# Kernel tuning notes

Hardware: AMD Instinct MI355X
Metric: run time of the kernel (lower is better)

## Reference

```python
import jax, jax.numpy as jnp
import numpy as np

NUM_GRAPHS = 64  # number of graphs in the batch for global_mean_pool
BN_EPS = 1e-5


def setup_inputs() -> dict:
    key = jax.random.key(0)
    ks = jax.random.split(key, 8)
    N, E, D, H, O = 100000, 1600000, 128, 128, 32
    x = jax.random.normal(ks[0], (N, D), dtype=jnp.float32)
    edge_index = jax.random.randint(ks[1], (2, E), 0, N, dtype=jnp.int64)
    batch = jnp.sort(jax.random.randint(ks[2], (N,), 0, NUM_GRAPHS, dtype=jnp.int64))
    s = 1.0 / np.sqrt(D)
    W0 = (jax.random.normal(ks[3], (D, H), dtype=jnp.float32) * s)
    b0 = jnp.zeros((H,), jnp.float32)
    g0 = jnp.ones((H,), jnp.float32)
    be0 = jnp.zeros((H,), jnp.float32)
    W1 = (jax.random.normal(ks[4], (H, H), dtype=jnp.float32) * s)
    b1 = jnp.zeros((H,), jnp.float32)
    g1 = jnp.ones((H,), jnp.float32)
    be1 = jnp.zeros((H,), jnp.float32)
    Wfc = (jax.random.normal(ks[5], (H, O), dtype=jnp.float32) * s)
    bfc = jnp.zeros((O,), jnp.float32)
    return dict(x=x, edge_index=edge_index, batch=batch,
                W0=W0, b0=b0, g0=g0, be0=be0,
                W1=W1, b1=b1, g1=g1, be1=be1,
                Wfc=Wfc, bfc=bfc)


def reference(x, edge_index, batch, W0, b0, g0, be0, W1, b1, g1, be1, Wfc, bfc):
    N = x.shape[0]
    loops = jnp.arange(N, dtype=edge_index.dtype)
    src = jnp.concatenate([edge_index[0], loops])  # [E+N]
    dst = jnp.concatenate([edge_index[1], loops])
    # GCN symmetric normalization on A + I
    deg = jax.ops.segment_sum(jnp.ones_like(dst, jnp.float32), dst, num_segments=N)
    dinv = jnp.where(deg > 0, jax.lax.rsqrt(deg), 0.0)
    norm = dinv[src] * dinv[dst]  # [E+N]

    def gcn_layer(h, W, b):
        h = h @ W                                   # [N, H] transform first (PyG GCNConv)
        msg = h[src] * norm[:, None]                # gather + scale
        agg = jax.ops.segment_sum(msg, dst, num_segments=N)  # scatter-add
        return agg + b

    def bn_relu(h, g, be):  # BatchNorm1d (batch stats, biased var) + ReLU
        mu = h.mean(axis=0)
        var = h.var(axis=0)
        return jax.nn.relu((h - mu) * jax.lax.rsqrt(var + BN_EPS) * g + be)

    h = bn_relu(gcn_layer(x, W0, b0), g0, be0)
    h = bn_relu(gcn_layer(h, W1, b1), g1, be1)

    # global_mean_pool over graph assignment
    cnt = jax.ops.segment_sum(jnp.ones((N,), jnp.float32), batch, num_segments=NUM_GRAPHS)
    pooled = jax.ops.segment_sum(h, batch, num_segments=NUM_GRAPHS)
    pooled = pooled / jnp.maximum(cnt, 1.0)[:, None]
    return pooled @ Wfc + bfc  # [NUM_GRAPHS, out_dim]
```

## Files before the change

kernel.cpp:

```cpp
#include <hip/hip_runtime.h>

typedef short bf16x8 __attribute__((ext_vector_type(8)));
typedef float f32x4 __attribute__((ext_vector_type(4)));

#define NBLK 512
#define NSTAT 512

__device__ __forceinline__ unsigned short f2bf(float f) {
    unsigned u = __float_as_uint(f);
    u += 0x7fffu + ((u >> 16) & 1u);
    return (unsigned short)(u >> 16);
}
__device__ __forceinline__ float bflo(unsigned u) { return __uint_as_float(u << 16); }
__device__ __forceinline__ float bfhi(unsigned u) { return __uint_as_float(u & 0xffff0000u); }


__global__ __launch_bounds__(256) void kb_count(const int* __restrict__ dst, int E, int nb,
                                                int chunk, int* __restrict__ counts) {
    __shared__ int h[512];
    for (int i = threadIdx.x; i < 512; i += 256) h[i] = 0;
    __syncthreads();
    int e0 = blockIdx.x * chunk, e1 = min(e0 + chunk, E);
    for (int e = e0 + threadIdx.x; e < e1; e += 256) atomicAdd(&h[dst[e] >> 8], 1);
    __syncthreads();
    for (int b = threadIdx.x; b < nb; b += 256) counts[b * NBLK + blockIdx.x] = h[b];
}

__global__ __launch_bounds__(NBLK) void kb_offsets(int* __restrict__ counts,
                                                   int* __restrict__ total) {
    __shared__ int s[NBLK];
    int b = blockIdx.x, t = threadIdx.x;
    int v = counts[b * NBLK + t];
    s[t] = v; __syncthreads();
    for (int off = 1; off < NBLK; off <<= 1) {
        int x = (t >= off) ? s[t - off] : 0;
        __syncthreads();
        s[t] += x;
        __syncthreads();
    }
    counts[b * NBLK + t] = s[t] - v;
    if (t == NBLK - 1) total[b] = s[t];
}

__global__ __launch_bounds__(512) void kb_base(const int* __restrict__ in, int nb,
                                               int* __restrict__ outb) {
    __shared__ int s[512];
    int t = threadIdx.x;
    int v = (t < nb) ? in[t] : 0;
    s[t] = v; __syncthreads();
    for (int off = 1; off < 512; off <<= 1) {
        int x = (t >= off) ? s[t - off] : 0;
        __syncthreads();
        s[t] += x;
        __syncthreads();
    }
    if (t < nb) outb[t] = s[t] - v;
}

__global__ __launch_bounds__(NBLK) void kb_scatter(const int* __restrict__ src,
                                                   const int* __restrict__ dst, int E, int nb,
                                                   int chunk,
                                                   const int* __restrict__ counts,
                                                   const int* __restrict__ bbase,
                                                   int2* __restrict__ rec) {
    __shared__ int cur[512];
    int t = threadIdx.x;
    if (t < nb) cur[t] = bbase[t] + counts[t * NBLK + blockIdx.x];
    __syncthreads();
    int e0 = blockIdx.x * chunk, e1 = min(e0 + chunk, E);
    for (int e = e0 + t; e < e1; e += NBLK) {
        int s = src[e], d = dst[e];
        int pos = atomicAdd(&cur[d >> 8], 1);
        rec[pos] = make_int2(s, d);
    }
}

__global__ __launch_bounds__(256) void kb_deg(const int2* __restrict__ rec,
                                              const int* __restrict__ bbase,
                                              const int* __restrict__ total,
                                              int* __restrict__ deg,
                                              float* __restrict__ dinv,
                                              int* __restrict__ padsum, int N) {
    __shared__ int dc[256];
    int b = blockIdx.x, t = threadIdx.x;
    dc[t] = 0; __syncthreads();
    int r0 = bbase[b], r1 = r0 + total[b];
    for (int i = r0 + t; i < r1; i += 256) atomicAdd(&dc[rec[i].y & 255], 1);
    __syncthreads();
    int gn = b * 256 + t;
    int d = dc[t];
    int pd = (gn < N) ? ((d + 7) & ~7) : 0;
    if (gn < N) {
        deg[gn] = d;
        dinv[gn] = rsqrtf((float)(d + 1));
    }
    __syncthreads();
    dc[t] = pd; __syncthreads();
    for (int off = 128; off > 0; off >>= 1) {
        if (t < off) dc[t] += dc[t + off];
        __syncthreads();
    }
    if (t == 0) padsum[b] = dc[0];
}

__global__ __launch_bounds__(256) void kb_place(const int2* __restrict__ rec,
                                                const int* __restrict__ bbase,
                                                const int* __restrict__ total,
                                                const int* __restrict__ bucketBase,
                                                const int* __restrict__ deg,
                                                const float* __restrict__ dinv,
                                                int2* __restrict__ csr,
                                                int2* __restrict__ rowdeg, int N) {
    __shared__ int sc[256];
    __shared__ int cur[256];
    int b = blockIdx.x, t = threadIdx.x;
    int gn = b * 256 + t;
    int d = (gn < N) ? deg[gn] : 0;
    int pd = (d + 7) & ~7;
    sc[t] = pd; __syncthreads();
    for (int off = 1; off < 256; off <<= 1) {
        int x = (t >= off) ? sc[t - off] : 0;
        __syncthreads();
        sc[t] += x;
        __syncthreads();
    }
    int rp = bucketBase[b] + sc[t] - pd;
    if (gn < N) rowdeg[gn] = make_int2(rp, pd);
    cur[t] = rp;
    __syncthreads();
    int r0 = bbase[b], r1 = r0 + total[b];
    for (int i = r0 + t; i < r1; i += 256) {
        int2 rc = rec[i];
        int pos = atomicAdd(&cur[rc.y & 255], 1);
        float w = dinv[rc.x] * dinv[rc.y];
        csr[pos] = make_int2(rc.x, __float_as_int(w));
    }
    __syncthreads();
    if (gn < N) {
        int end = cur[t];
        int pe = rp + pd;
        for (int i = end; i < pe; ++i) csr[i] = make_int2(0, 0);
    }
}

__global__ __launch_bounds__(256) void k_wprep(const float* __restrict__ W0,
                                               const float* __restrict__ W1,
                                               unsigned short* __restrict__ W0t,
                                               unsigned short* __restrict__ W1t,
                                               float* __restrict__ pooled,
                                               int* __restrict__ gcnt) {
    int tt = blockIdx.x * 256 + threadIdx.x;
    pooled[tt] = 0.f;
    pooled[tt + 4096] = 0.f;
    if (tt < 64) gcnt[tt] = 0;
    const float* W = (tt < 2048) ? W0 : W1;
    unsigned short* Wt = (tt < 2048) ? W0t : W1t;
    int t = tt & 2047;
    int f = t >> 6, lane = t & 63;
    int kc = f >> 3, nt = f & 7;
    int kbase = kc * 32 + (lane >> 4) * 8;
    int n = nt * 16 + (lane & 15);
    unsigned short t8[8];
#pragma unroll
    for (int j = 0; j < 8; ++j) t8[j] = f2bf(W[(size_t)(kbase + j) * 128 + n]);
    unsigned short* o = &Wt[(size_t)t * 8];
    *(ushort4*)&o[0] = *(ushort4*)&t8[0];
    *(ushort4*)&o[4] = *(ushort4*)&t8[4];
}

__global__ __launch_bounds__(256) void k_gemm(const void* __restrict__ Xv,
                                              const unsigned short* __restrict__ Wt,
                                              const float* __restrict__ scale,
                                              const float* __restrict__ shift,
                                              unsigned short* __restrict__ Hout,
                                              int N, int xbf16) {
    __shared__ unsigned short sX[64 * 136];
    const int tid = threadIdx.x;
    const int rowBase = blockIdx.x * 64;

    if (!xbf16) {
        const float* X = (const float*)Xv;
#pragma unroll
        for (int i = 0; i < 8; ++i) {
            int f4 = tid + 256 * i;
            int r = f4 >> 5; int k4 = (f4 & 31) * 4;
            int gr = rowBase + r;
            float4 v = make_float4(0.f, 0.f, 0.f, 0.f);
            if (gr < N) v = *(const float4*)&X[(size_t)gr * 128 + k4];
            ushort4 p;
            p.x = f2bf(v.x); p.y = f2bf(v.y); p.z = f2bf(v.z); p.w = f2bf(v.w);
            *(ushort4*)&sX[r * 136 + k4] = p;
        }
    } else {
        const int4* X = (const int4*)Xv;
#pragma unroll
        for (int i = 0; i < 4; ++i) {
            int f8 = tid + 256 * i;
            int r = f8 >> 4; int k8 = (f8 & 15) * 8;
            int gr = rowBase + r;
            int4 u = make_int4(0, 0, 0, 0);
            if (gr < N) u = X[(size_t)gr * 16 + (f8 & 15)];
            float fv[8] = { bflo(u.x), bfhi(u.x), bflo(u.y), bfhi(u.y),
                            bflo(u.z), bfhi(u.z), bflo(u.w), bfhi(u.w) };
            unsigned short t8[8];
#pragma unroll
            for (int j = 0; j < 8; ++j)
                t8[j] = f2bf(fmaxf(fmaf(fv[j], scale[k8 + j], shift[k8 + j]), 0.f));
            *(ushort4*)&sX[r * 136 + k8]     = *(ushort4*)&t8[0];
            *(ushort4*)&sX[r * 136 + k8 + 4] = *(ushort4*)&t8[4];
        }
    }
    __syncthreads();

    const int lane = tid & 63, wave = tid >> 6;
    const int m = lane & 15, q = lane >> 4;
    const int rowOff = (wave * 16 + m) * 136 + q * 8;
    f32x4 acc[8];
#pragma unroll
    for (int nt = 0; nt < 8; ++nt) acc[nt] = (f32x4){0.f, 0.f, 0.f, 0.f};
    const bf16x8* WtF = (const bf16x8*)Wt;
#pragma unroll
    for (int kc = 0; kc < 4; ++kc) {
        bf16x8 xb = *(const bf16x8*)&sX[rowOff + kc * 32];
#pragma unroll
        for (int nt = 0; nt < 8; ++nt) {
            bf16x8 wa = WtF[(kc * 8 + nt) * 64 + lane];
            acc[nt] = __builtin_amdgcn_mfma_f32_16x16x32_bf16(wa, xb, acc[nt], 0, 0, 0);
        }
    }
    int grow = rowBase + wave * 16 + m;
    if (grow < N) {
#pragma unroll
        for (int nt = 0; nt < 8; ++nt) {
            ushort4 p;
            p.x = f2bf(acc[nt][0]); p.y = f2bf(acc[nt][1]);
            p.z = f2bf(acc[nt][2]); p.w = f2bf(acc[nt][3]);
            *(ushort4*)&Hout[(size_t)grow * 128 + nt * 16 + q * 4] = p;
        }
    }
}

__global__ __launch_bounds__(256) void k_agg(const unsigned short* __restrict__ H,
                                             const int2* __restrict__ rowdeg,
                                             const int2* __restrict__ csr,
                                             const float* __restrict__ dinv,
                                             const float* __restrict__ bias,
                                             unsigned* __restrict__ out, int N) {
    int wave = threadIdx.x >> 6;
    int lane = threadIdx.x & 63;
    int node = blockIdx.x * 4 + wave;
    if (node >= N) return;
    const unsigned* Hu = (const unsigned*)H;
    int2 rd = rowdeg[node];
    int start = rd.x, pd = rd.y;
    float a0 = 0.f, a1 = 0.f;
    const int4* cp = (const int4*)(csr + start);
    int j = 0;
    for (; j + 16 <= pd; j += 16) {
        int4 q0 = cp[0], q1 = cp[1], q2 = cp[2], q3 = cp[3];
        int4 q4 = cp[4], q5 = cp[5], q6 = cp[6], q7 = cp[7];
        cp += 8;
        unsigned u0 = Hu[(size_t)q0.x * 64 + lane];
        unsigned u1 = Hu[(size_t)q0.z * 64 + lane];
        unsigned u2 = Hu[(size_t)q1.x * 64 + lane];
        unsigned u3 = Hu[(size_t)q1.z * 64 + lane];
        unsigned u4 = Hu[(size_t)q2.x * 64 + lane];
        unsigned u5 = Hu[(size_t)q2.z * 64 + lane];
        unsigned u6 = Hu[(size_t)q3.x * 64 + lane];
        unsigned u7 = Hu[(size_t)q3.z * 64 + lane];
        unsigned u8 = Hu[(size_t)q4.x * 64 + lane];
        unsigned u9 = Hu[(size_t)q4.z * 64 + lane];
        unsigned uA = Hu[(size_t)q5.x * 64 + lane];
        unsigned uB = Hu[(size_t)q5.z * 64 + lane];
        unsigned uC = Hu[(size_t)q6.x * 64 + lane];
        unsigned uD = Hu[(size_t)q6.z * 64 + lane];
        unsigned uE = Hu[(size_t)q7.x * 64 + lane];
        unsigned uF = Hu[(size_t)q7.z * 64 + lane];
        float w0 = __int_as_float(q0.y), w1 = __int_as_float(q0.w);
        float w2 = __int_as_float(q1.y), w3 = __int_as_float(q1.w);
        float w4 = __int_as_float(q2.y), w5 = __int_as_float(q2.w);
        float w6 = __int_as_float(q3.y), w7 = __int_as_float(q3.w);
        float w8 = __int_as_float(q4.y), w9 = __int_as_float(q4.w);
        float wA = __int_as_float(q5.y), wB = __int_as_float(q5.w);
        float wC = __int_as_float(q6.y), wD = __int_as_float(q6.w);
        float wE = __int_as_float(q7.y), wF = __int_as_float(q7.w);
        a0 = fmaf(w0, bflo(u0), a0); a1 = fmaf(w0, bfhi(u0), a1);
        a0 = fmaf(w1, bflo(u1), a0); a1 = fmaf(w1, bfhi(u1), a1);
        a0 = fmaf(w2, bflo(u2), a0); a1 = fmaf(w2, bfhi(u2), a1);
        a0 = fmaf(w3, bflo(u3), a0); a1 = fmaf(w3, bfhi(u3), a1);
        a0 = fmaf(w4, bflo(u4), a0); a1 = fmaf(w4, bfhi(u4), a1);
        a0 = fmaf(w5, bflo(u5), a0); a1 = fmaf(w5, bfhi(u5), a1);
        a0 = fmaf(w6, bflo(u6), a0); a1 = fmaf(w6, bfhi(u6), a1);
        a0 = fmaf(w7, bflo(u7), a0); a1 = fmaf(w7, bfhi(u7), a1);
        a0 = fmaf(w8, bflo(u8), a0); a1 = fmaf(w8, bfhi(u8), a1);
        a0 = fmaf(w9, bflo(u9), a0); a1 = fmaf(w9, bfhi(u9), a1);
        a0 = fmaf(wA, bflo(uA), a0); a1 = fmaf(wA, bfhi(uA), a1);
        a0 = fmaf(wB, bflo(uB), a0); a1 = fmaf(wB, bfhi(uB), a1);
        a0 = fmaf(wC, bflo(uC), a0); a1 = fmaf(wC, bfhi(uC), a1);
        a0 = fmaf(wD, bflo(uD), a0); a1 = fmaf(wD, bfhi(uD), a1);
        a0 = fmaf(wE, bflo(uE), a0); a1 = fmaf(wE, bfhi(uE), a1);
        a0 = fmaf(wF, bflo(uF), a0); a1 = fmaf(wF, bfhi(uF), a1);
    }
    if (j < pd) {
        int4 q0 = cp[0], q1 = cp[1], q2 = cp[2], q3 = cp[3];
        unsigned u0 = Hu[(size_t)q0.x * 64 + lane];
        unsigned u1 = Hu[(size_t)q0.z * 64 + lane];
        unsigned u2 = Hu[(size_t)q1.x * 64 + lane];
        unsigned u3 = Hu[(size_t)q1.z * 64 + lane];
        unsigned u4 = Hu[(size_t)q2.x * 64 + lane];
        unsigned u5 = Hu[(size_t)q2.z * 64 + lane];
        unsigned u6 = Hu[(size_t)q3.x * 64 + lane];
        unsigned u7 = Hu[(size_t)q3.z * 64 + lane];
        float w0 = __int_as_float(q0.y), w1 = __int_as_float(q0.w);
        float w2 = __int_as_float(q1.y), w3 = __int_as_float(q1.w);
        float w4 = __int_as_float(q2.y), w5 = __int_as_float(q2.w);
        float w6 = __int_as_float(q3.y), w7 = __int_as_float(q3.w);
        a0 = fmaf(w0, bflo(u0), a0); a1 = fmaf(w0, bfhi(u0), a1);
        a0 = fmaf(w1, bflo(u1), a0); a1 = fmaf(w1, bfhi(u1), a1);
        a0 = fmaf(w2, bflo(u2), a0); a1 = fmaf(w2, bfhi(u2), a1);
        a0 = fmaf(w3, bflo(u3), a0); a1 = fmaf(w3, bfhi(u3), a1);
        a0 = fmaf(w4, bflo(u4), a0); a1 = fmaf(w4, bfhi(u4), a1);
        a0 = fmaf(w5, bflo(u5), a0); a1 = fmaf(w5, bfhi(u5), a1);
        a0 = fmaf(w6, bflo(u6), a0); a1 = fmaf(w6, bfhi(u6), a1);
        a0 = fmaf(w7, bflo(u7), a0); a1 = fmaf(w7, bfhi(u7), a1);
    }
    {
        float dn = dinv[node];
        float w = dn * dn;
        unsigned u = Hu[(size_t)node * 64 + lane];
        a0 = fmaf(w, bflo(u), a0);
        a1 = fmaf(w, bfhi(u), a1);
    }
    float2 bv = ((const float2*)bias)[lane];
    a0 += bv.x; a1 += bv.y;
    out[(size_t)node * 64 + lane] = (unsigned)f2bf(a0) | ((unsigned)f2bf(a1) << 16);
}

__global__ __launch_bounds__(256) void k_stats(const int4* __restrict__ B4, int N,
                                               float* __restrict__ P1,
                                               float* __restrict__ P2) {
    int tid = threadIdx.x;
    int lane = tid & 63, wave = tid >> 6;
    int c = lane & 15;
    int rsub = lane >> 4;
    float s1[8] = {0.f,0.f,0.f,0.f,0.f,0.f,0.f,0.f};
    float s2[8] = {0.f,0.f,0.f,0.f,0.f,0.f,0.f,0.f};
    for (int r = blockIdx.x * 16 + wave * 4 + rsub; r < N; r += NSTAT * 16) {
        int4 u = B4[(size_t)r * 16 + c];
        float f[8] = { bflo(u.x), bfhi(u.x), bflo(u.y), bfhi(u.y),
                       bflo(u.z), bfhi(u.z), bflo(u.w), bfhi(u.w) };
#pragma unroll
        for (int j = 0; j < 8; ++j) { s1[j] += f[j]; s2[j] = fmaf(f[j], f[j], s2[j]); }
    }
#pragma unroll
    for (int j = 0; j < 8; ++j) {
        s1[j] += __shfl_xor(s1[j], 16, 64);
        s1[j] += __shfl_xor(s1[j], 32, 64);
        s2[j] += __shfl_xor(s2[j], 16, 64);
        s2[j] += __shfl_xor(s2[j], 32, 64);
    }
    __shared__ float ls1[4][128], ls2[4][128];
    if (rsub == 0) {
#pragma unroll
        for (int j = 0; j < 8; ++j) { ls1[wave][c * 8 + j] = s1[j]; ls2[wave][c * 8 + j] = s2[j]; }
    }
    __syncthreads();
    if (tid < 128) {
        P1[blockIdx.x * 128 + tid] = ls1[0][tid] + ls1[1][tid] + ls1[2][tid] + ls1[3][tid];
        P2[blockIdx.x * 128 + tid] = ls2[0][tid] + ls2[1][tid] + ls2[2][tid] + ls2[3][tid];
    }
}

__global__ __launch_bounds__(256) void k_bnfinal(const float* __restrict__ P1,
                          const float* __restrict__ P2,
                          const float* __restrict__ g, const float* __restrict__ be,
                          float* __restrict__ scale, float* __restrict__ shift,
                          float invN, int nPart) {
    int f = blockIdx.x, t = threadIdx.x;
    float s1 = 0.f, s2 = 0.f;
    for (int i = t; i < nPart; i += 256) {
        s1 += P1[(size_t)i * 128 + f];
        s2 += P2[(size_t)i * 128 + f];
    }
    __shared__ float l1[256], l2[256];
    l1[t] = s1; l2[t] = s2;
    __syncthreads();
    for (int off = 128; off > 0; off >>= 1) {
        if (t < off) { l1[t] += l1[t + off]; l2[t] += l2[t + off]; }
        __syncthreads();
    }
    if (t == 0) {
        float mu = l1[0] * invN;
        float var = l2[0] * invN - mu * mu;
        float sc = g[f] * rsqrtf(var + 1e-5f);
        scale[f] = sc;
        shift[f] = fmaf(-mu, sc, be[f]);
    }
}

__global__ __launch_bounds__(256) void k_pool(const int4* __restrict__ B4,
                                              const float* __restrict__ scale,
                                              const float* __restrict__ shift,
                                              const int* __restrict__ batch, int N,
                                              int rpb, float* __restrict__ pooled,
                                              int* __restrict__ gcnt) {
    __shared__ float lp[64 * 128];
    __shared__ int lc[64];
    int tid = threadIdx.x;
    int r0 = blockIdx.x * rpb;
    int r1 = min(r0 + rpb, N);
    int g0 = batch[r0];
    int g1 = batch[r1 - 1];
    for (int i = g0 * 128 + tid; i < (g1 + 1) * 128; i += 256) lp[i] = 0.f;
    if (tid <= g1 - g0) lc[g0 + tid] = 0;
    __syncthreads();

    int c = tid & 15;
    int rh = tid >> 4;
    float sc[8], sh[8];
#pragma unroll
    for (int j = 0; j < 8; ++j) { sc[j] = scale[c * 8 + j]; sh[j] = shift[c * 8 + j]; }
    float acc[8] = {0.f,0.f,0.f,0.f,0.f,0.f,0.f,0.f};
    int cnt = 0;
    int cur = -1;
    for (int r = r0 + rh; r < r1; r += 16) {
        int g = batch[r];
        if (g != cur) {
            if (cur >= 0) {
#pragma unroll
                for (int j = 0; j < 8; ++j)
                    atomicAdd(&lp[cur * 128 + c * 8 + j], acc[j]);
                if (c == 0) atomicAdd(&lc[cur], cnt);
            }
#pragma unroll
            for (int j = 0; j < 8; ++j) acc[j] = 0.f;
            cnt = 0;
            cur = g;
        }
        int4 u = B4[(size_t)r * 16 + c];
        float f[8] = { bflo(u.x), bfhi(u.x), bflo(u.y), bfhi(u.y),
                       bflo(u.z), bfhi(u.z), bflo(u.w), bfhi(u.w) };
#pragma unroll
        for (int j = 0; j < 8; ++j) acc[j] += fmaxf(fmaf(f[j], sc[j], sh[j]), 0.f);
        ++cnt;
    }
    if (cur >= 0) {
#pragma unroll
        for (int j = 0; j < 8; ++j)
            atomicAdd(&lp[cur * 128 + c * 8 + j], acc[j]);
        if (c == 0) atomicAdd(&lc[cur], cnt);
    }
    __syncthreads();
    for (int i = g0 * 128 + tid; i < (g1 + 1) * 128; i += 256) {
        float v = lp[i];
        if (v != 0.f) atomicAdd(&pooled[i], v);
    }
    if (tid <= g1 - g0) {
        int v = lc[g0 + tid];
        if (v) atomicAdd(&gcnt[g0 + tid], v);
    }
}

__global__ __launch_bounds__(256) void k_fc(const float* __restrict__ pooled,
                                            const int* __restrict__ gcnt,
                                            const float* __restrict__ Wfc,
                                            const float* __restrict__ bfc,
                                            float* __restrict__ out) {
    int idx = blockIdx.x * 256 + threadIdx.x;
    if (idx >= 64 * 32) return;
    int g = idx >> 5, o = idx & 31;
    float inv = 1.f / fmaxf((float)gcnt[g], 1.f);
    float acc = bfc[o];
    for (int k = 0; k < 128; ++k)
        acc = fmaf(pooled[g * 128 + k] * inv, Wfc[k * 32 + o], acc);
    out[idx] = acc;
}

extern "C" void kernel_launch(void* const* d_in, const int* in_sizes, int n_in,
                              void* d_out, int out_size, void* d_ws, size_t ws_size,
                              hipStream_t stream) {
    const float* x    = (const float*)d_in[0];
    const int*  eidx  = (const int*)d_in[1];
    const int*  batch = (const int*)d_in[2];
    const float* W0 = (const float*)d_in[3];
    const float* b0 = (const float*)d_in[4];
    const float* g0 = (const float*)d_in[5];
    const float* be0 = (const float*)d_in[6];
    const float* W1 = (const float*)d_in[7];
    const float* b1 = (const float*)d_in[8];
    const float* g1 = (const float*)d_in[9];
    const float* be1 = (const float*)d_in[10];
    const float* Wfc = (const float*)d_in[11];
    const float* bfc = (const float*)d_in[12];
    float* out = (float*)d_out;

    const int N = in_sizes[0] / 128;
    const int E = in_sizes[1] / 2;
    const int* esrc = eidx;
    const int* edst = eidx + E;
    const int NB = (N + 255) >> 8;
    const size_t paddedE = (size_t)E + 7 * (size_t)N;

    char* base = (char*)d_ws;
    size_t off = 0;
    auto take = [&](size_t bytes) -> char* {
        char* p = base + off;
        off = (off + bytes + 255) & ~(size_t)255;
        return p;
    };
    unsigned short* hA = (unsigned short*)take((size_t)N * 128 * 2);
    int2* rec = (int2*)hA;
    unsigned* B = (unsigned*)take((size_t)N * 64 * 4);
    int2* csr   = (int2*)take(paddedE * 8);
    int2* rowdeg = (int2*)take((size_t)N * 8);
    int* deg    = (int*)take((size_t)N * 4);
    float* dinv = (float*)take((size_t)N * 4);
    int* counts = (int*)take((size_t)512 * NBLK * 4);
    int* total  = (int*)take(512 * 4);
    int* bbase  = (int*)take(512 * 4);
    int* padsum = (int*)take(512 * 4);
    int* bucketBase = (int*)take(512 * 4);
    unsigned short* W0t = (unsigned short*)take(16384 * 2);
    unsigned short* W1t = (unsigned short*)take(16384 * 2);
    float* P1 = (float*)take((size_t)NSTAT * 128 * 4);
    float* P2 = (float*)take((size_t)NSTAT * 128 * 4);
    float* pooled = (float*)take(64 * 128 * 4);
    int*   gcnt   = (int*)take(64 * 4);
    float* scale1 = (float*)take(128 * 4);
    float* shift1 = (float*)take(128 * 4);
    float* scale2 = (float*)take(128 * 4);
    float* shift2 = (float*)take(128 * 4);
    (void)ws_size; (void)n_in; (void)out_size;

    k_wprep<<<16, 256, 0, stream>>>(W0, W1, W0t, W1t, pooled, gcnt);

    const int CH256 = (E + NBLK - 1) / NBLK;
    kb_count<<<NBLK, 256, 0, stream>>>(edst, E, NB, CH256, counts);
    kb_offsets<<<NB, NBLK, 0, stream>>>(counts, total);
    kb_base<<<1, 512, 0, stream>>>(total, NB, bbase);
    kb_scatter<<<NBLK, NBLK, 0, stream>>>(esrc, edst, E, NB, CH256, counts, bbase, rec);
    kb_deg<<<NB, 256, 0, stream>>>(rec, bbase, total, deg, dinv, padsum, N);
    kb_base<<<1, 512, 0, stream>>>(padsum, NB, bucketBase);
    kb_place<<<NB, 256, 0, stream>>>(rec, bbase, total, bucketBase, deg, dinv, csr, rowdeg, N);

    const int gGemm = (N + 63) / 64;
    const int gAgg  = (N + 3) / 4;
    const float invN = 1.0f / (float)N;

    k_gemm<<<gGemm, 256, 0, stream>>>(x, W0t, scale1, shift1, hA, N, 0);
    k_agg<<<gAgg, 256, 0, stream>>>(hA, rowdeg, csr, dinv, b0, B, N);
    k_stats<<<NSTAT, 256, 0, stream>>>((const int4*)B, N, P1, P2);
    k_bnfinal<<<128, 256, 0, stream>>>(P1, P2, g0, be0, scale1, shift1, invN, NSTAT);

    k_gemm<<<gGemm, 256, 0, stream>>>(B, W1t, scale1, shift1, hA, N, 1);
    k_agg<<<gAgg, 256, 0, stream>>>(hA, rowdeg, csr, dinv, b1, B, N);
    k_stats<<<NSTAT, 256, 0, stream>>>((const int4*)B, N, P1, P2);
    k_bnfinal<<<128, 256, 0, stream>>>(P1, P2, g1, be1, scale2, shift2, invN, NSTAT);

    const int rpb = (N + 511) / 512;
    k_pool<<<(N + rpb - 1) / rpb, 256, 0, stream>>>((const int4*)B, scale2, shift2, batch, N, rpb, pooled, gcnt);
    k_fc<<<8, 256, 0, stream>>>(pooled, gcnt, Wfc, bfc, out);
}
```

Baseline: 378.3 us.

## Cut kernel launches by fusing scans, stats finalization, and first GEMM with scatter

Removes the two single-block scan kernels by having each consumer block recompute its prefix from the totals. The layer-0 GEMM now runs as extra blocks inside the edge-scatter kernel, so the two overlap. BatchNorm finalization and the FC head move into last-block-done epilogues of the stats and pool kernels, guarded by atomic counters. The CSR reads in aggregation use nontemporal loads. The aim is fewer launches and less serialization, in exchange for redundant prefix work per block and reliance on threadfence and counter ordering.

```diff
diff --git a/kernel.cpp b/kernel.cpp
--- a/kernel.cpp
+++ b/kernel.cpp
@@ -2,6 +2,7 @@
 
 typedef short bf16x8 __attribute__((ext_vector_type(8)));
 typedef float f32x4 __attribute__((ext_vector_type(4)));
+typedef int   i32x4 __attribute__((ext_vector_type(4)));
 
 #define NBLK 512
 #define NSTAT 512
@@ -14,6 +15,34 @@
 __device__ __forceinline__ float bflo(unsigned u) { return __uint_as_float(u << 16); }
 __device__ __forceinline__ float bfhi(unsigned u) { return __uint_as_float(u & 0xffff0000u); }
 
+__global__ __launch_bounds__(256) void k_wprep(const float* __restrict__ W0,
+                                               const float* __restrict__ W1,
+                                               unsigned short* __restrict__ W0t,
+                                               unsigned short* __restrict__ W1t,
+                                               float* __restrict__ pooled,
+                                               int* __restrict__ gcnt,
+                                               int* __restrict__ cnt,
+                                               int* __restrict__ total) {
+    int tt = blockIdx.x * 256 + threadIdx.x;
+    pooled[tt] = 0.f;
+    pooled[tt + 4096] = 0.f;
+    if (tt < 64) gcnt[tt] = 0;
+    if (tt < 4) cnt[tt] = 0;
+    if (tt < 512) total[tt] = 0;
+    const float* W = (tt < 2048) ? W0 : W1;
+    unsigned short* Wt = (tt < 2048) ? W0t : W1t;
+    int t = tt & 2047;
+    int f = t >> 6, lane = t & 63;
+    int kc = f >> 3, nt = f & 7;
+    int kbase = kc * 32 + (lane >> 4) * 8;
+    int n = nt * 16 + (lane & 15);
+    unsigned short t8[8];
+#pragma unroll
+    for (int j = 0; j < 8; ++j) t8[j] = f2bf(W[(size_t)(kbase + j) * 128 + n]);
+    unsigned short* o = &Wt[(size_t)t * 8];
+    *(ushort4*)&o[0] = *(ushort4*)&t8[0];
+    *(ushort4*)&o[4] = *(ushort4*)&t8[4];
+}
 
 __global__ __launch_bounds__(256) void kb_count(const int* __restrict__ dst, int E, int nb,
                                                 int chunk, int* __restrict__ counts) {
@@ -42,49 +71,98 @@
     if (t == NBLK - 1) total[b] = s[t];
 }
 
-__global__ __launch_bounds__(512) void kb_base(const int* __restrict__ in, int nb,
-                                               int* __restrict__ outb) {
-    __shared__ int s[512];
-    int t = threadIdx.x;
-    int v = (t < nb) ? in[t] : 0;
-    s[t] = v; __syncthreads();
-    for (int off = 1; off < 512; off <<= 1) {
-        int x = (t >= off) ? s[t - off] : 0;
-        __syncthreads();
-        s[t] += x;
-        __syncthreads();
-    }
-    if (t < nb) outb[t] = s[t] - v;
-}
-
-__global__ __launch_bounds__(NBLK) void kb_scatter(const int* __restrict__ src,
-                                                   const int* __restrict__ dst, int E, int nb,
-                                                   int chunk,
-                                                   const int* __restrict__ counts,
-                                                   const int* __restrict__ bbase,
-                                                   int2* __restrict__ rec) {
-    __shared__ int cur[512];
-    int t = threadIdx.x;
-    if (t < nb) cur[t] = bbase[t] + counts[t * NBLK + blockIdx.x];
-    __syncthreads();
-    int e0 = blockIdx.x * chunk, e1 = min(e0 + chunk, E);
-    for (int e = e0 + t; e < e1; e += NBLK) {
-        int s = src[e], d = dst[e];
-        int pos = atomicAdd(&cur[d >> 8], 1);
-        rec[pos] = make_int2(s, d);
+__global__ __launch_bounds__(256) void k_scatgemm(const int* __restrict__ src,
+                                                  const int* __restrict__ dst, int E, int chunk,
+                                                  const int* __restrict__ counts,
+                                                  const int* __restrict__ total,
+                                                  int2* __restrict__ rec,
+                                                  const float* __restrict__ X,
+                                                  const unsigned short* __restrict__ Wt,
+                                                  unsigned short* __restrict__ Hout, int N) {
+    __shared__ unsigned short smem[64 * 136];
+    const int t = threadIdx.x;
+    if (blockIdx.x < NBLK) {
+        int* sS  = (int*)smem;
+        int* cur = ((int*)smem) + 512;
+        sS[t] = total[t]; sS[t + 256] = total[t + 256];
+        __syncthreads();
+        for (int off = 1; off < 512; off <<= 1) {
+            int a  = (t >= off) ? sS[t - off] : 0;
+            int b2 = (t + 256 >= off) ? sS[t + 256 - off] : 0;
+            __syncthreads();
+            sS[t] += a; sS[t + 256] += b2;
+            __syncthreads();
+        }
+        int blk = blockIdx.x;
+        cur[t]       = sS[t] - total[t] + counts[t * NBLK + blk];
+        cur[t + 256] = sS[t + 256] - total[t + 256] + counts[(t + 256) * NBLK + blk];
+        __syncthreads();
+        int e0 = blk * chunk, e1 = min(e0 + chunk, E);
+        for (int e = e0 + t; e < e1; e += 256) {
+            int s = src[e], d = dst[e];
+            int pos = atomicAdd(&cur[d >> 8], 1);
+            rec[pos] = make_int2(s, d);
+        }
+    } else {
+        const int rowBase = (blockIdx.x - NBLK) * 64;
+#pragma unroll
+        for (int i = 0; i < 8; ++i) {
+            int f4 = t + 256 * i;
+            int r = f4 >> 5; int k4 = (f4 & 31) * 4;
+            int gr = rowBase + r;
+            float4 v = make_float4(0.f, 0.f, 0.f, 0.f);
+            if (gr < N) v = *(const float4*)&X[(size_t)gr * 128 + k4];
+            ushort4 p;
+            p.x = f2bf(v.x); p.y = f2bf(v.y); p.z = f2bf(v.z); p.w = f2bf(v.w);
+            *(ushort4*)&smem[r * 136 + k4] = p;
+        }
+        __syncthreads();
+        const int lane = t & 63, wave = t >> 6;
+        const int m = lane & 15, q = lane >> 4;
+        const int rowOff = (wave * 16 + m) * 136 + q * 8;
+        f32x4 acc[8];
+#pragma unroll
+        for (int nt = 0; nt < 8; ++nt) acc[nt] = (f32x4){0.f, 0.f, 0.f, 0.f};
+        const bf16x8* WtF = (const bf16x8*)Wt;
+#pragma unroll
+        for (int kc = 0; kc < 4; ++kc) {
+            bf16x8 xb = *(const bf16x8*)&smem[rowOff + kc * 32];
+#pragma unroll
+            for (int nt = 0; nt < 8; ++nt) {
+                bf16x8 wa = WtF[(kc * 8 + nt) * 64 + lane];
+                acc[nt] = __builtin_amdgcn_mfma_f32_16x16x32_bf16(wa, xb, acc[nt], 0, 0, 0);
+            }
+        }
+        int grow = rowBase + wave * 16 + m;
+        if (grow < N) {
+#pragma unroll
+            for (int nt = 0; nt < 8; ++nt) {
+                ushort4 p;
+                p.x = f2bf(acc[nt][0]); p.y = f2bf(acc[nt][1]);
+                p.z = f2bf(acc[nt][2]); p.w = f2bf(acc[nt][3]);
+                *(ushort4*)&Hout[(size_t)grow * 128 + nt * 16 + q * 4] = p;
+            }
+        }
     }
 }
 
 __global__ __launch_bounds__(256) void kb_deg(const int2* __restrict__ rec,
-                                              const int* __restrict__ bbase,
                                               const int* __restrict__ total,
                                               int* __restrict__ deg,
                                               float* __restrict__ dinv,
                                               int* __restrict__ padsum, int N) {
     __shared__ int dc[256];
+    __shared__ int red[256];
     int b = blockIdx.x, t = threadIdx.x;
-    dc[t] = 0; __syncthreads();
-    int r0 = bbase[b], r1 = r0 + total[b];
+    red[t] = ((t < b) ? total[t] : 0) + ((t + 256 < b) ? total[t + 256] : 0);
+    dc[t] = 0;
+    __syncthreads();
+    for (int off = 128; off > 0; off >>= 1) {
+        if (t < off) red[t] += red[t + off];
+        __syncthreads();
+    }
+    int r0 = red[0];
+    int r1 = r0 + total[b];
     for (int i = r0 + t; i < r1; i += 256) atomicAdd(&dc[rec[i].y & 255], 1);
     __syncthreads();
     int gn = b * 256 + t;
@@ -104,16 +182,27 @@
 }
 
 __global__ __launch_bounds__(256) void kb_place(const int2* __restrict__ rec,
-                                                const int* __restrict__ bbase,
                                                 const int* __restrict__ total,
-                                                const int* __restrict__ bucketBase,
+                                                const int* __restrict__ padsum,
                                                 const int* __restrict__ deg,
                                                 const float* __restrict__ dinv,
                                                 int2* __restrict__ csr,
                                                 int2* __restrict__ rowdeg, int N) {
     __shared__ int sc[256];
     __shared__ int cur[256];
+    __shared__ int red[256];
     int b = blockIdx.x, t = threadIdx.x;
+    red[t] = ((t < b) ? total[t]  : 0) + ((t + 256 < b) ? total[t + 256]  : 0);
+    sc[t]  = ((t < b) ? padsum[t] : 0) + ((t + 256 < b) ? padsum[t + 256] : 0);
+    __syncthreads();
+    for (int off = 128; off > 0; off >>= 1) {
+        if (t < off) { red[t] += red[t + off]; sc[t] += sc[t + off]; }
+        __syncthreads();
+    }
+    int r0 = red[0];
+    int r1 = r0 + total[b];
+    int bucketBase = sc[0];
+    __syncthreads();
     int gn = b * 256 + t;
     int d = (gn < N) ? deg[gn] : 0;
     int pd = (d + 7) & ~7;
@@ -124,11 +213,10 @@
         sc[t] += x;
         __syncthreads();
     }
-    int rp = bucketBase[b] + sc[t] - pd;
+    int rp = bucketBase + sc[t] - pd;
     if (gn < N) rowdeg[gn] = make_int2(rp, pd);
     cur[t] = rp;
     __syncthreads();
-    int r0 = bbase[b], r1 = r0 + total[b];
     for (int i = r0 + t; i < r1; i += 256) {
         int2 rc = rec[i];
         int pos = atomicAdd(&cur[rc.y & 255], 1);
@@ -143,75 +231,31 @@
     }
 }
 
-__global__ __launch_bounds__(256) void k_wprep(const float* __restrict__ W0,
-                                               const float* __restrict__ W1,
-                                               unsigned short* __restrict__ W0t,
-                                               unsigned short* __restrict__ W1t,
-                                               float* __restrict__ pooled,
-                                               int* __restrict__ gcnt) {
-    int tt = blockIdx.x * 256 + threadIdx.x;
-    pooled[tt] = 0.f;
-    pooled[tt + 4096] = 0.f;
-    if (tt < 64) gcnt[tt] = 0;
-    const float* W = (tt < 2048) ? W0 : W1;
-    unsigned short* Wt = (tt < 2048) ? W0t : W1t;
-    int t = tt & 2047;
-    int f = t >> 6, lane = t & 63;
-    int kc = f >> 3, nt = f & 7;
-    int kbase = kc * 32 + (lane >> 4) * 8;
-    int n = nt * 16 + (lane & 15);
-    unsigned short t8[8];
-#pragma unroll
-    for (int j = 0; j < 8; ++j) t8[j] = f2bf(W[(size_t)(kbase + j) * 128 + n]);
-    unsigned short* o = &Wt[(size_t)t * 8];
-    *(ushort4*)&o[0] = *(ushort4*)&t8[0];
-    *(ushort4*)&o[4] = *(ushort4*)&t8[4];
-}
-
-__global__ __launch_bounds__(256) void k_gemm(const void* __restrict__ Xv,
+__global__ __launch_bounds__(256) void k_gemm(const int4* __restrict__ X,
                                               const unsigned short* __restrict__ Wt,
                                               const float* __restrict__ scale,
                                               const float* __restrict__ shift,
-                                              unsigned short* __restrict__ Hout,
-                                              int N, int xbf16) {
+                                              unsigned short* __restrict__ Hout, int N) {
     __shared__ unsigned short sX[64 * 136];
     const int tid = threadIdx.x;
     const int rowBase = blockIdx.x * 64;
-
-    if (!xbf16) {
-        const float* X = (const float*)Xv;
-#pragma unroll
-        for (int i = 0; i < 8; ++i) {
-            int f4 = tid + 256 * i;
-            int r = f4 >> 5; int k4 = (f4 & 31) * 4;
-            int gr = rowBase + r;
-            float4 v = make_float4(0.f, 0.f, 0.f, 0.f);
-            if (gr < N) v = *(const float4*)&X[(size_t)gr * 128 + k4];
-            ushort4 p;
-            p.x = f2bf(v.x); p.y = f2bf(v.y); p.z = f2bf(v.z); p.w = f2bf(v.w);
-            *(ushort4*)&sX[r * 136 + k4] = p;
-        }
-    } else {
-        const int4* X = (const int4*)Xv;
-#pragma unroll
-        for (int i = 0; i < 4; ++i) {
-            int f8 = tid + 256 * i;
-            int r = f8 >> 4; int k8 = (f8 & 15) * 8;
-            int gr = rowBase + r;
-            int4 u = make_int4(0, 0, 0, 0);
-            if (gr < N) u = X[(size_t)gr * 16 + (f8 & 15)];
-            float fv[8] = { bflo(u.x), bfhi(u.x), bflo(u.y), bfhi(u.y),
-                            bflo(u.z), bfhi(u.z), bflo(u.w), bfhi(u.w) };
-            unsigned short t8[8];
-#pragma unroll
-            for (int j = 0; j < 8; ++j)
-                t8[j] = f2bf(fmaxf(fmaf(fv[j], scale[k8 + j], shift[k8 + j]), 0.f));
-            *(ushort4*)&sX[r * 136 + k8]     = *(ushort4*)&t8[0];
-            *(ushort4*)&sX[r * 136 + k8 + 4] = *(ushort4*)&t8[4];
-        }
-    }
-    __syncthreads();
-
+#pragma unroll
+    for (int i = 0; i < 4; ++i) {
+        int f8 = tid + 256 * i;
+        int r = f8 >> 4; int k8 = (f8 & 15) * 8;
+        int gr = rowBase + r;
+        int4 u = make_int4(0, 0, 0, 0);
+        if (gr < N) u = X[(size_t)gr * 16 + (f8 & 15)];
+        float fv[8] = { bflo(u.x), bfhi(u.x), bflo(u.y), bfhi(u.y),
+                        bflo(u.z), bfhi(u.z), bflo(u.w), bfhi(u.w) };
+        unsigned short t8[8];
+#pragma unroll
+        for (int j = 0; j < 8; ++j)
+            t8[j] = f2bf(fmaxf(fmaf(fv[j], scale[k8 + j], shift[k8 + j]), 0.f));
+        *(ushort4*)&sX[r * 136 + k8]     = *(ushort4*)&t8[0];
+        *(ushort4*)&sX[r * 136 + k8 + 4] = *(ushort4*)&t8[4];
+    }
+    __syncthreads();
     const int lane = tid & 63, wave = tid >> 6;
     const int m = lane & 15, q = lane >> 4;
     const int rowOff = (wave * 16 + m) * 136 + q * 8;
@@ -254,36 +298,42 @@
     int2 rd = rowdeg[node];
     int start = rd.x, pd = rd.y;
     float a0 = 0.f, a1 = 0.f;
-    const int4* cp = (const int4*)(csr + start);
+    const i32x4* cp = (const i32x4*)(csr + start);
     int j = 0;
     for (; j + 16 <= pd; j += 16) {
-        int4 q0 = cp[0], q1 = cp[1], q2 = cp[2], q3 = cp[3];
-        int4 q4 = cp[4], q5 = cp[5], q6 = cp[6], q7 = cp[7];
+        i32x4 q0 = __builtin_nontemporal_load(cp + 0);
+        i32x4 q1 = __builtin_nontemporal_load(cp + 1);
+        i32x4 q2 = __builtin_nontemporal_load(cp + 2);
+        i32x4 q3 = __builtin_nontemporal_load(cp + 3);
+        i32x4 q4 = __builtin_nontemporal_load(cp + 4);
+        i32x4 q5 = __builtin_nontemporal_load(cp + 5);
+        i32x4 q6 = __builtin_nontemporal_load(cp + 6);
+        i32x4 q7 = __builtin_nontemporal_load(cp + 7);
         cp += 8;
-        unsigned u0 = Hu[(size_t)q0.x * 64 + lane];
-        unsigned u1 = Hu[(size_t)q0.z * 64 + lane];
-        unsigned u2 = Hu[(size_t)q1.x * 64 + lane];
-        unsigned u3 = Hu[(size_t)q1.z * 64 + lane];
-        unsigned u4 = Hu[(size_t)q2.x * 64 + lane];
-        unsigned u5 = Hu[(size_t)q2.z * 64 + lane];
-        unsigned u6 = Hu[(size_t)q3.x * 64 + lane];
-        unsigned u7 = Hu[(size_t)q3.z * 64 + lane];
-        unsigned u8 = Hu[(size_t)q4.x * 64 + lane];
-        unsigned u9 = Hu[(size_t)q4.z * 64 + lane];
-        unsigned uA = Hu[(size_t)q5.x * 64 + lane];
-        unsigned uB = Hu[(size_t)q5.z * 64 + lane];
-        unsigned uC = Hu[(size_t)q6.x * 64 + lane];
-        unsigned uD = Hu[(size_t)q6.z * 64 + lane];
-        unsigned uE = Hu[(size_t)q7.x * 64 + lane];
-        unsigned uF = Hu[(size_t)q7.z * 64 + lane];
-        float w0 = __int_as_float(q0.y), w1 = __int_as_float(q0.w);
-        float w2 = __int_as_float(q1.y), w3 = __int_as_float(q1.w);
-        float w4 = __int_as_float(q2.y), w5 = __int_as_float(q2.w);
-        float w6 = __int_as_float(q3.y), w7 = __int_as_float(q3.w);
-        float w8 = __int_as_float(q4.y), w9 = __int_as_float(q4.w);
-        float wA = __int_as_float(q5.y), wB = __int_as_float(q5.w);
-        float wC = __int_as_float(q6.y), wD = __int_as_float(q6.w);
-        float wE = __int_as_float(q7.y), wF = __int_as_float(q7.w);
+        unsigned u0 = Hu[(size_t)q0[0] * 64 + lane];
+        unsigned u1 = Hu[(size_t)q0[2] * 64 + lane];
+        unsigned u2 = Hu[(size_t)q1[0] * 64 + lane];
+        unsigned u3 = Hu[(size_t)q1[2] * 64 + lane];
+        unsigned u4 = Hu[(size_t)q2[0] * 64 + lane];
+        unsigned u5 = Hu[(size_t)q2[2] * 64 + lane];
+        unsigned u6 = Hu[(size_t)q3[0] * 64 + lane];
+        unsigned u7 = Hu[(size_t)q3[2] * 64 + lane];
+        unsigned u8 = Hu[(size_t)q4[0] * 64 + lane];
+        unsigned u9 = Hu[(size_t)q4[2] * 64 + lane];
+        unsigned uA = Hu[(size_t)q5[0] * 64 + lane];
+        unsigned uB = Hu[(size_t)q5[2] * 64 + lane];
+        unsigned uC = Hu[(size_t)q6[0] * 64 + lane];
+        unsigned uD = Hu[(size_t)q6[2] * 64 + lane];
+        unsigned uE = Hu[(size_t)q7[0] * 64 + lane];
+        unsigned uF = Hu[(size_t)q7[2] * 64 + lane];
+        float w0 = __int_as_float(q0[1]), w1 = __int_as_float(q0[3]);
+        float w2 = __int_as_float(q1[1]), w3 = __int_as_float(q1[3]);
+        float w4 = __int_as_float(q2[1]), w5 = __int_as_float(q2[3]);
+        float w6 = __int_as_float(q3[1]), w7 = __int_as_float(q3[3]);
+        float w8 = __int_as_float(q4[1]), w9 = __int_as_float(q4[3]);
+        float wA = __int_as_float(q5[1]), wB = __int_as_float(q5[3]);
+        float wC = __int_as_float(q6[1]), wD = __int_as_float(q6[3]);
+        float wE = __int_as_float(q7[1]), wF = __int_as_float(q7[3]);
         a0 = fmaf(w0, bflo(u0), a0); a1 = fmaf(w0, bfhi(u0), a1);
         a0 = fmaf(w1, bflo(u1), a0); a1 = fmaf(w1, bfhi(u1), a1);
         a0 = fmaf(w2, bflo(u2), a0); a1 = fmaf(w2, bfhi(u2), a1);
@@ -302,19 +352,22 @@
         a0 = fmaf(wF, bflo(uF), a0); a1 = fmaf(wF, bfhi(uF), a1);
     }
     if (j < pd) {
-        int4 q0 = cp[0], q1 = cp[1], q2 = cp[2], q3 = cp[3];
-        unsigned u0 = Hu[(size_t)q0.x * 64 + lane];
-        unsigned u1 = Hu[(size_t)q0.z * 64 + lane];
-        unsigned u2 = Hu[(size_t)q1.x * 64 + lane];
-        unsigned u3 = Hu[(size_t)q1.z * 64 + lane];
-        unsigned u4 = Hu[(size_t)q2.x * 64 + lane];
-        unsigned u5 = Hu[(size_t)q2.z * 64 + lane];
-        unsigned u6 = Hu[(size_t)q3.x * 64 + lane];
-        unsigned u7 = Hu[(size_t)q3.z * 64 + lane];
-        float w0 = __int_as_float(q0.y), w1 = __int_as_float(q0.w);
-        float w2 = __int_as_float(q1.y), w3 = __int_as_float(q1.w);
-        float w4 = __int_as_float(q2.y), w5 = __int_as_float(q2.w);
-        float w6 = __int_as_float(q3.y), w7 = __int_as_float(q3.w);
+        i32x4 q0 = __builtin_nontemporal_load(cp + 0);
+        i32x4 q1 = __builtin_nontemporal_load(cp + 1);
+        i32x4 q2 = __builtin_nontemporal_load(cp + 2);
+        i32x4 q3 = __builtin_nontemporal_load(cp + 3);
+        unsigned u0 = Hu[(size_t)q0[0] * 64 + lane];
+        unsigned u1 = Hu[(size_t)q0[2] * 64 + lane];
+        unsigned u2 = Hu[(size_t)q1[0] * 64 + lane];
+        unsigned u3 = Hu[(size_t)q1[2] * 64 + lane];
+        unsigned u4 = Hu[(size_t)q2[0] * 64 + lane];
+        unsigned u5 = Hu[(size_t)q2[2] * 64 + lane];
+        unsigned u6 = Hu[(size_t)q3[0] * 64 + lane];
+        unsigned u7 = Hu[(size_t)q3[2] * 64 + lane];
+        float w0 = __int_as_float(q0[1]), w1 = __int_as_float(q0[3]);
+        float w2 = __int_as_float(q1[1]), w3 = __int_as_float(q1[3]);
+        float w4 = __int_as_float(q2[1]), w5 = __int_as_float(q2[3]);
+        float w6 = __int_as_float(q3[1]), w7 = __int_as_float(q3[3]);
         a0 = fmaf(w0, bflo(u0), a0); a1 = fmaf(w0, bfhi(u0), a1);
         a0 = fmaf(w1, bflo(u1), a0); a1 = fmaf(w1, bfhi(u1), a1);
         a0 = fmaf(w2, bflo(u2), a0); a1 = fmaf(w2, bfhi(u2), a1);
@@ -333,12 +386,18 @@
     }
     float2 bv = ((const float2*)bias)[lane];
     a0 += bv.x; a1 += bv.y;
-    out[(size_t)node * 64 + lane] = (unsigned)f2bf(a0) | ((unsigned)f2bf(a1) << 16);
+    unsigned pk = (unsigned)f2bf(a0) | ((unsigned)f2bf(a1) << 16);
+    __builtin_nontemporal_store(pk, &out[(size_t)node * 64 + lane]);
 }
 
 __global__ __launch_bounds__(256) void k_stats(const int4* __restrict__ B4, int N,
                                                float* __restrict__ P1,
-                                               float* __restrict__ P2) {
+                                               float* __restrict__ P2,
+                                               const float* __restrict__ g,
+                                               const float* __restrict__ be,
+                                               float* __restrict__ scale,
+                                               float* __restrict__ shift,
+                                               float invN, int* __restrict__ counter) {
     int tid = threadIdx.x;
     int lane = tid & 63, wave = tid >> 6;
     int c = lane & 15;
@@ -369,32 +428,26 @@
         P1[blockIdx.x * 128 + tid] = ls1[0][tid] + ls1[1][tid] + ls1[2][tid] + ls1[3][tid];
         P2[blockIdx.x * 128 + tid] = ls2[0][tid] + ls2[1][tid] + ls2[2][tid] + ls2[3][tid];
     }
-}
-
-__global__ __launch_bounds__(256) void k_bnfinal(const float* __restrict__ P1,
-                          const float* __restrict__ P2,
-                          const float* __restrict__ g, const float* __restrict__ be,
-                          float* __restrict__ scale, float* __restrict__ shift,
-                          float invN, int nPart) {
-    int f = blockIdx.x, t = threadIdx.x;
-    float s1 = 0.f, s2 = 0.f;
-    for (int i = t; i < nPart; i += 256) {
-        s1 += P1[(size_t)i * 128 + f];
-        s2 += P2[(size_t)i * 128 + f];
-    }
-    __shared__ float l1[256], l2[256];
-    l1[t] = s1; l2[t] = s2;
-    __syncthreads();
-    for (int off = 128; off > 0; off >>= 1) {
-        if (t < off) { l1[t] += l1[t + off]; l2[t] += l2[t + off]; }
-        __syncthreads();
-    }
-    if (t == 0) {
-        float mu = l1[0] * invN;
-        float var = l2[0] * invN - mu * mu;
-        float sc = g[f] * rsqrtf(var + 1e-5f);
-        scale[f] = sc;
-        shift[f] = fmaf(-mu, sc, be[f]);
+    __threadfence();
+    __shared__ int isLast;
+    if (tid == 0) isLast = (atomicAdd(counter, 1) == (int)gridDim.x - 1);
+    __syncthreads();
+    if (!isLast) return;
+    __threadfence();
+    int f = tid & 127;
+    const float* P = (tid < 128) ? P1 : P2;
+    float s = 0.f;
+#pragma unroll 8
+    for (int i = 0; i < NSTAT; ++i) s += P[i * 128 + f];
+    __shared__ float sm[256];
+    sm[tid] = s;
+    __syncthreads();
+    if (tid < 128) {
+        float mu = sm[tid] * invN;
+        float var = sm[tid + 128] * invN - mu * mu;
+        float sc = g[tid] * rsqrtf(var + 1e-5f);
+        scale[tid] = sc;
+        shift[tid] = fmaf(-mu, sc, be[tid]);
     }
 }
 
@@ -403,7 +456,11 @@
                                               const float* __restrict__ shift,
                                               const int* __restrict__ batch, int N,
                                               int rpb, float* __restrict__ pooled,
-                                              int* __restrict__ gcnt) {
+                                              int* __restrict__ gcnt,
+                                              const float* __restrict__ Wfc,
+                                              const float* __restrict__ bfc,
+                                              float* __restrict__ out,
+                                              int* __restrict__ counter) {
     __shared__ float lp[64 * 128];
     __shared__ int lc[64];
     int tid = threadIdx.x;
@@ -459,21 +516,20 @@
         int v = lc[g0 + tid];
         if (v) atomicAdd(&gcnt[g0 + tid], v);
     }
-}
-
-__global__ __launch_bounds__(256) void k_fc(const float* __restrict__ pooled,
-                                            const int* __restrict__ gcnt,
-                                            const float* __restrict__ Wfc,
-                                            const float* __restrict__ bfc,
-                                            float* __restrict__ out) {
-    int idx = blockIdx.x * 256 + threadIdx.x;
-    if (idx >= 64 * 32) return;
-    int g = idx >> 5, o = idx & 31;
-    float inv = 1.f / fmaxf((float)gcnt[g], 1.f);
-    float acc = bfc[o];
-    for (int k = 0; k < 128; ++k)
-        acc = fmaf(pooled[g * 128 + k] * inv, Wfc[k * 32 + o], acc);
-    out[idx] = acc;
+    __threadfence();
+    __shared__ int isLast;
+    if (tid == 0) isLast = (atomicAdd(counter, 1) == (int)gridDim.x - 1);
+    __syncthreads();
+    if (!isLast) return;
+    __threadfence();
+    for (int idx = tid; idx < 64 * 32; idx += 256) {
+        int g = idx >> 5, o = idx & 31;
+        float inv = 1.f / fmaxf((float)gcnt[g], 1.f);
+        float a = bfc[o];
+        for (int k = 0; k < 128; ++k)
+            a = fmaf(pooled[g * 128 + k] * inv, Wfc[k * 32 + o], a);
+        out[idx] = a;
+    }
 }
 
 extern "C" void kernel_launch(void* const* d_in, const int* in_sizes, int n_in,
@@ -509,17 +565,16 @@
         return p;
     };
     unsigned short* hA = (unsigned short*)take((size_t)N * 128 * 2);
-    int2* rec = (int2*)hA;
     unsigned* B = (unsigned*)take((size_t)N * 64 * 4);
+    int2* rec = (int2*)B;
     int2* csr   = (int2*)take(paddedE * 8);
     int2* rowdeg = (int2*)take((size_t)N * 8);
     int* deg    = (int*)take((size_t)N * 4);
     float* dinv = (float*)take((size_t)N * 4);
     int* counts = (int*)take((size_t)512 * NBLK * 4);
     int* total  = (int*)take(512 * 4);
-    int* bbase  = (int*)take(512 * 4);
     int* padsum = (int*)take(512 * 4);
-    int* bucketBase = (int*)take(512 * 4);
+    int* cntrs  = (int*)take(4 * 4);
     unsigned short* W0t = (unsigned short*)take(16384 * 2);
     unsigned short* W1t = (unsigned short*)take(16384 * 2);
     float* P1 = (float*)take((size_t)NSTAT * 128 * 4);
@@ -532,32 +587,28 @@
     float* shift2 = (float*)take(128 * 4);
     (void)ws_size; (void)n_in; (void)out_size;
 
-    k_wprep<<<16, 256, 0, stream>>>(W0, W1, W0t, W1t, pooled, gcnt);
-
-    const int CH256 = (E + NBLK - 1) / NBLK;
-    kb_count<<<NBLK, 256, 0, stream>>>(edst, E, NB, CH256, counts);
-    kb_offsets<<<NB, NBLK, 0, stream>>>(counts, total);
-    kb_base<<<1, 512, 0, stream>>>(total, NB, bbase);
-    kb_scatter<<<NBLK, NBLK, 0, stream>>>(esrc, edst, E, NB, CH256, counts, bbase, rec);
-    kb_deg<<<NB, 256, 0, stream>>>(rec, bbase, total, deg, dinv, padsum, N);
-    kb_base<<<1, 512, 0, stream>>>(padsum, NB, bucketBase);
-    kb_place<<<NB, 256, 0, stream>>>(rec, bbase, total, bucketBase, deg, dinv, csr, rowdeg, N);
-
     const int gGemm = (N + 63) / 64;
     const int gAgg  = (N + 3) / 4;
     const float invN = 1.0f / (float)N;
-
-    k_gemm<<<gGemm, 256, 0, stream>>>(x, W0t, scale1, shift1, hA, N, 0);
+    const int CH = (E + NBLK - 1) / NBLK;
+
+    k_wprep<<<16, 256, 0, stream>>>(W0, W1, W0t, W1t, pooled, gcnt, cntrs, total);
+    kb_count<<<NBLK, 256, 0, stream>>>(edst, E, NB, CH, counts);
+    kb_offsets<<<NB, NBLK, 0, stream>>>(counts, total);
+    k_scatgemm<<<NBLK + gGemm, 256, 0, stream>>>(esrc, edst, E, CH, counts, total,
+                                                 rec, x, W0t, hA, N);
+    kb_deg<<<NB, 256, 0, stream>>>(rec, total, deg, dinv, padsum, N);
+    kb_place<<<NB, 256, 0, stream>>>(rec, total, padsum, deg, dinv, csr, rowdeg, N);
+
     k_agg<<<gAgg, 256, 0, stream>>>(hA, rowdeg, csr, dinv, b0, B, N);
-    k_stats<<<NSTAT, 256, 0, stream>>>((const int4*)B, N, P1, P2);
-    k_bnfinal<<<128, 256, 0, stream>>>(P1, P2, g0, be0, scale1, shift1, invN, NSTAT);
-
-    k_gemm<<<gGemm, 256, 0, stream>>>(B, W1t, scale1, shift1, hA, N, 1);
+    k_stats<<<NSTAT, 256, 0, stream>>>((const int4*)B, N, P1, P2, g0, be0,
+                                       scale1, shift1, invN, cntrs + 0);
+    k_gemm<<<gGemm, 256, 0, stream>>>((const int4*)B, W1t, scale1, shift1, hA, N);
     k_agg<<<gAgg, 256, 0, stream>>>(hA, rowdeg, csr, dinv, b1, B, N);
-    k_stats<<<NSTAT, 256, 0, stream>>>((const int4*)B, N, P1, P2);
-    k_bnfinal<<<128, 256, 0, stream>>>(P1, P2, g1, be1, scale2, shift2, invN, NSTAT);
-
+    k_stats<<<NSTAT, 256, 0, stream>>>((const int4*)B, N, P1, P2, g1, be1,
+                                       scale2, shift2, invN, cntrs + 1);
     const int rpb = (N + 511) / 512;
-    k_pool<<<(N + rpb - 1) / rpb, 256, 0, stream>>>((const int4*)B, scale2, shift2, batch, N, rpb, pooled, gcnt);
-    k_fc<<<8, 256, 0, stream>>>(pooled, gcnt, Wfc, bfc, out);
-}
+    k_pool<<<(N + rpb - 1) / rpb, 256, 0, stream>>>((const int4*)B, scale2, shift2,
+                                                    batch, N, rpb, pooled, gcnt,
+                                                    Wfc, bfc, out, cntrs + 2);
+}
```

After: 530.8 us. 40.3% more time.
